# Kernel tuning notes

Hardware: AMD Instinct MI355X
Metric: run time of the kernel (lower is better)

## Reference

```python
import jax, jax.numpy as jnp
import numpy as np

B = 262144
N_USERS = 100000
N_LOCS = 2000
N_ISBNS = 100000
SBERT_DIM = 384
NUM_CATS = 64
EMB = 48
TEMP = 0.05
ALPHA = 3.0
BETA = 1.0


def setup_inputs() -> dict:
    key = jax.random.key(0)
    ks = jax.random.split(key, 20)
    s = 0.05
    inp = {
        "user_idx": jax.random.randint(ks[0], (B,), 0, N_USERS),
        "loc_idx": jax.random.randint(ks[1], (B,), 0, N_LOCS),
        "pos_idx": jax.random.randint(ks[2], (B,), 0, N_ISBNS),
        "neg_idx": jax.random.randint(ks[3], (B,), 0, N_ISBNS),
        "user_cat_emb": jax.random.normal(ks[4], (N_USERS, EMB), jnp.float32) * s,
        "user_txt_emb": jax.random.normal(ks[5], (N_USERS, EMB), jnp.float32) * s,
        "loc_cat_emb": jax.random.normal(ks[6], (N_LOCS, EMB), jnp.float32) * s,
        "loc_txt_emb": jax.random.normal(ks[7], (N_LOCS, EMB), jnp.float32) * s,
        "sbert_matrix": jax.random.normal(ks[8], (N_ISBNS, SBERT_DIM), jnp.float32) * s,
        # multi-hot category matrix (~3 categories per book on average)
        "book_cat_mh": (jax.random.uniform(ks[9], (N_ISBNS, NUM_CATS)) < 0.05).astype(jnp.float32),
        "Wc1": jax.random.normal(ks[10], (NUM_CATS, 128), jnp.float32) * s,
        "bc1": jnp.zeros((128,), jnp.float32),
        "Wc2": jax.random.normal(ks[11], (128, EMB), jnp.float32) * s,
        "bc2": jnp.zeros((EMB,), jnp.float32),
        "Wt1": jax.random.normal(ks[12], (SBERT_DIM, 256), jnp.float32) * s,
        "bt1": jnp.zeros((256,), jnp.float32),
        "Wt2": jax.random.normal(ks[13], (256, EMB), jnp.float32) * s,
        "bt2": jnp.zeros((EMB,), jnp.float32),
    }
    return inp


def _l2norm(x):
    # tf.nn.l2_normalize: x / sqrt(max(sum(x^2), eps)), eps=1e-12
    sq = jnp.sum(x * x, axis=-1, keepdims=True)
    return x * jax.lax.rsqrt(jnp.maximum(sq, 1e-12))


def _encode_book(idx, sbert_matrix, book_cat_mh, Wc1, bc1, Wc2, bc2, Wt1, bt1, Wt2, bt2):
    b_cat_in = book_cat_mh[idx]                      # [B, NUM_CATS]
    b_txt_in = sbert_matrix[idx]                     # [B, SBERT_DIM]
    b_cat = jax.nn.relu(b_cat_in @ Wc1 + bc1) @ Wc2 + bc2   # [B, EMB]
    b_txt = jax.nn.relu(b_txt_in @ Wt1 + bt1) @ Wt2 + bt2   # [B, EMB]
    return _l2norm(ALPHA * b_cat + BETA * b_txt)


def reference(user_idx, loc_idx, pos_idx, neg_idx,
              user_cat_emb, user_txt_emb, loc_cat_emb, loc_txt_emb,
              sbert_matrix, book_cat_mh,
              Wc1, bc1, Wc2, bc2, Wt1, bt1, Wt2, bt2):
    # user tower (dropout inactive at inference)
    u = ALPHA * (user_cat_emb[user_idx] + loc_cat_emb[loc_idx]) \
        + BETA * (user_txt_emb[user_idx] + loc_txt_emb[loc_idx])
    u = _l2norm(u)
    p = _encode_book(pos_idx, sbert_matrix, book_cat_mh, Wc1, bc1, Wc2, bc2, Wt1, bt1, Wt2, bt2)
    n = _encode_book(neg_idx, sbert_matrix, book_cat_mh, Wc1, bc1, Wc2, bc2, Wt1, bt1, Wt2, bt2)
    pos_sim = jnp.sum(u * p, axis=-1) / TEMP
    neg_sim = jnp.sum(u * n, axis=-1) / TEMP
    return jnp.stack([pos_sim, neg_sim], axis=-1)  # [B, 2]
```

## Files before the change

### kernel.cpp

```cpp
#include <hip/hip_runtime.h>

#define SBD   384
#define NCATS 64
#define EMB   48
#define HT    256
#define HC    128
#define MB    64

typedef __attribute__((ext_vector_type(8))) short short8;
typedef __attribute__((ext_vector_type(4))) float f32x4;

__device__ __forceinline__ short f2bf(float x) {
    union { float f; unsigned u; } v; v.f = x;
    unsigned r = v.u + 0x7FFF + ((v.u >> 16) & 1);
    return (short)(r >> 16);
}

__device__ __forceinline__ void glds16(const void* g, void* l) {
    __builtin_amdgcn_global_load_lds((const __attribute__((address_space(1))) void*)g,
                                     (__attribute__((address_space(3))) void*)l, 16, 0, 0);
}

__global__ void prep_weights(const float* __restrict__ Wt1, const float* __restrict__ Wt2,
                             const float* __restrict__ Wc1, const float* __restrict__ Wc2,
                             char* __restrict__ iT1, char* __restrict__ iT2,
                             char* __restrict__ iC1, char* __restrict__ iC2) {
    int t = blockIdx.x * blockDim.x + threadIdx.x;
    int stride = gridDim.x * blockDim.x;
    for (int g = t; g < 256 * 48; g += stride) {
        int n = g / 48, k0 = (g - n * 48) * 8;
        int c = k0 >> 5, kin = k0 & 31;
        short8 v;
        #pragma unroll
        for (int j = 0; j < 8; ++j) v[j] = f2bf(Wt1[(size_t)(k0 + j) * HT + n]);
        *(short8*)(iT1 + (size_t)c * 16384 + ((n * 64 + kin * 2) ^ ((n & 7) << 4))) = v;
    }
    for (int g = t; g < 48 * 32; g += stride) {
        int n = g / 32, k0 = (g - n * 32) * 8;
        short8 v;
        #pragma unroll
        for (int j = 0; j < 8; ++j) v[j] = f2bf(Wt2[(size_t)(k0 + j) * EMB + n]);
        *(short8*)(iT2 + ((n * 512 + k0 * 2) ^ ((n & 7) << 4))) = v;
    }
    for (int g = t; g < 128 * 8; g += stride) {
        int n = g / 8, k0 = (g - n * 8) * 8;
        short8 v;
        #pragma unroll
        for (int j = 0; j < 8; ++j) v[j] = f2bf(Wc1[(size_t)(k0 + j) * HC + n]);
        *(short8*)(iC1 + ((n * 128 + k0 * 2) ^ ((n & 7) << 4))) = v;
    }
    for (int g = t; g < 48 * 16; g += stride) {
        int n = g / 16, k0 = (g - n * 16) * 8;
        short8 v;
        #pragma unroll
        for (int j = 0; j < 8; ++j) v[j] = f2bf(Wc2[(size_t)(k0 + j) * EMB + n]);
        *(short8*)(iC2 + ((n * 256 + k0 * 2) ^ ((n & 7) << 4))) = v;
    }
}

__global__ __launch_bounds__(256, 2) void encode_books_mfma(
    const float* __restrict__ sbert, const float* __restrict__ mh,
    const char* __restrict__ iT1, const char* __restrict__ iT2,
    const char* __restrict__ iC1, const char* __restrict__ iC2,
    const float* __restrict__ bt1, const float* __restrict__ bt2,
    const float* __restrict__ bc1, const float* __restrict__ bc2,
    float* __restrict__ E, int nbooks)
{
    __shared__ char lds[73728];

    const int t  = threadIdx.x;
    const int w  = t >> 6;
    const int l  = t & 63;
    const int lr = l & 15;
    const int lg = l >> 4;
    const int book0 = blockIdx.x * MB;
    const int arow  = w * 16 + lr;
    const int drow0 = w * 16 + lg * 4;
    const int aswz  = (arow & 7) << 4;
    const int nswz  = (lr & 7) << 4;

    auto stageA = [&](int c, int buf) {
        int row = t >> 2, k0 = (t & 3) * 8;
        int rb = min(book0 + row, nbooks - 1);
        const float* s = sbert + (size_t)rb * SBD + c * 32 + k0;
        float4 v0 = *(const float4*)s, v1 = *(const float4*)(s + 4);
        short8 h;
        h[0] = f2bf(v0.x); h[1] = f2bf(v0.y); h[2] = f2bf(v0.z); h[3] = f2bf(v0.w);
        h[4] = f2bf(v1.x); h[5] = f2bf(v1.y); h[6] = f2bf(v1.z); h[7] = f2bf(v1.w);
        *(short8*)(lds + buf * 4096 + ((row * 64 + k0 * 2) ^ ((row & 7) << 4))) = h;
    };
    auto stageB = [&](const char* img, int dst, int bytes) {
        int perw = bytes >> 2;
        for (int i = 0; i < perw; i += 1024)
            glds16(img + w * perw + i + l * 16, lds + dst + w * perw + i);
    };

    f32x4 acc[16];
    #pragma unroll
    for (int nt = 0; nt < 16; ++nt) { float b = bt1[nt * 16 + lr]; acc[nt] = (f32x4){b, b, b, b}; }

    stageA(0, 0);
    stageB(iT1, 8192, 16384);
    __syncthreads();
    for (int c = 0; c < 12; ++c) {
        const int cur = c & 1;
        if (c < 11) {
            stageA(c + 1, cur ^ 1);
            stageB(iT1 + (size_t)(c + 1) * 16384, 8192 + (cur ^ 1) * 16384, 16384);
        }
        short8 af = *(const short8*)(lds + cur * 4096 + ((arow * 64 + lg * 16) ^ aswz));
        #pragma unroll
        for (int nt = 0; nt < 16; ++nt) {
            short8 bf = *(const short8*)(lds + 8192 + cur * 16384 +
                                         (((nt * 16 + lr) * 64 + lg * 16) ^ nswz));
            acc[nt] = __builtin_amdgcn_mfma_f32_16x16x32_bf16(af, bf, acc[nt], 0, 0, 0);
        }
        __syncthreads();
    }

    #pragma unroll
    for (int nt = 0; nt < 16; ++nt) {
        #pragma unroll
        for (int r = 0; r < 4; ++r) {
            int row = drow0 + r, col = nt * 16 + lr;
            *(unsigned short*)(lds + 40960 + ((row * 512 + col * 2) ^ ((row & 7) << 4))) =
                (unsigned short)f2bf(fmaxf(acc[nt][r], 0.f));
        }
    }
    stageB(iT2, 8192, 24576);
    #pragma unroll
    for (int i = 0; i < 2; ++i) {
        int g = t + 256 * i;
        int row = g >> 3, k0 = (g & 7) * 8;
        int rb = min(book0 + row, nbooks - 1);
        const float* s = mh + (size_t)rb * NCATS + k0;
        float4 v0 = *(const float4*)s, v1 = *(const float4*)(s + 4);
        short8 h;
        h[0] = f2bf(v0.x); h[1] = f2bf(v0.y); h[2] = f2bf(v0.z); h[3] = f2bf(v0.w);
        h[4] = f2bf(v1.x); h[5] = f2bf(v1.y); h[6] = f2bf(v1.z); h[7] = f2bf(v1.w);
        *(short8*)(lds + ((row * 128 + k0 * 2) ^ ((row & 7) << 4))) = h;
    }
    __syncthreads();

    f32x4 acct[3];
    #pragma unroll
    for (int nt = 0; nt < 3; ++nt) { float b = bt2[nt * 16 + lr]; acct[nt] = (f32x4){b, b, b, b}; }
    #pragma unroll
    for (int ks = 0; ks < 8; ++ks) {
        short8 af = *(const short8*)(lds + 40960 + ((arow * 512 + (lg * 8 + ks * 32) * 2) ^ aswz));
        #pragma unroll
        for (int nt = 0; nt < 3; ++nt) {
            short8 bf = *(const short8*)(lds + 8192 +
                (((nt * 16 + lr) * 512 + (lg * 8 + ks * 32) * 2) ^ nswz));
            acct[nt] = __builtin_amdgcn_mfma_f32_16x16x32_bf16(af, bf, acct[nt], 0, 0, 0);
        }
    }
    __syncthreads();

    stageB(iC1, 8192, 16384);
    stageB(iC2, 24576, 12288);
    __syncthreads();

    f32x4 accc[8];
    #pragma unroll
    for (int nt = 0; nt < 8; ++nt) { float b = bc1[nt * 16 + lr]; accc[nt] = (f32x4){b, b, b, b}; }
    #pragma unroll
    for (int ks = 0; ks < 2; ++ks) {
        short8 af = *(const short8*)(lds + ((arow * 128 + (lg * 8 + ks * 32) * 2) ^ aswz));
        #pragma unroll
        for (int nt = 0; nt < 8; ++nt) {
            short8 bf = *(const short8*)(lds + 8192 +
                (((nt * 16 + lr) * 128 + (lg * 8 + ks * 32) * 2) ^ nswz));
            accc[nt] = __builtin_amdgcn_mfma_f32_16x16x32_bf16(af, bf, accc[nt], 0, 0, 0);
        }
    }
    #pragma unroll
    for (int nt = 0; nt < 8; ++nt) {
        #pragma unroll
        for (int r = 0; r < 4; ++r) {
            int row = drow0 + r, col = nt * 16 + lr;
            *(unsigned short*)(lds + 40960 + ((row * 256 + col * 2) ^ ((row & 7) << 4))) =
                (unsigned short)f2bf(fmaxf(accc[nt][r], 0.f));
        }
    }
    __syncthreads();

    f32x4 acc2[3];
    #pragma unroll
    for (int nt = 0; nt < 3; ++nt) { float b = bc2[nt * 16 + lr]; acc2[nt] = (f32x4){b, b, b, b}; }
    #pragma unroll
    for (int ks = 0; ks < 4; ++ks) {
        short8 af = *(const short8*)(lds + 40960 + ((arow * 256 + (lg * 8 + ks * 32) * 2) ^ aswz));
        #pragma unroll
        for (int nt = 0; nt < 3; ++nt) {
            short8 bf = *(const short8*)(lds + 24576 +
                (((nt * 16 + lr) * 256 + (lg * 8 + ks * 32) * 2) ^ nswz));
            acc2[nt] = __builtin_amdgcn_mfma_f32_16x16x32_bf16(af, bf, acc2[nt], 0, 0, 0);
        }
    }

    f32x4 comb[3];
    #pragma unroll
    for (int nt = 0; nt < 3; ++nt)
        #pragma unroll
        for (int r = 0; r < 4; ++r) comb[nt][r] = 3.0f * acc2[nt][r] + acct[nt][r];
    float rn[4];
    #pragma unroll
    for (int r = 0; r < 4; ++r) {
        float ss = comb[0][r] * comb[0][r] + comb[1][r] * comb[1][r] + comb[2][r] * comb[2][r];
        ss += __shfl_xor(ss, 1); ss += __shfl_xor(ss, 2);
        ss += __shfl_xor(ss, 4); ss += __shfl_xor(ss, 8);
        rn[r] = rsqrtf(fmaxf(ss, 1e-12f));
    }
    #pragma unroll
    for (int nt = 0; nt < 3; ++nt) {
        #pragma unroll
        for (int r = 0; r < 4; ++r) {
            int grow = book0 + drow0 + r;
            if (grow < nbooks) E[(size_t)grow * EMB + nt * 16 + lr] = comb[nt][r] * rn[r];
        }
    }
}

__global__ __launch_bounds__(256) void score_kernel(
    const int* __restrict__ user_idx, const int* __restrict__ loc_idx,
    const int* __restrict__ pos_idx,  const int* __restrict__ neg_idx,
    const float* __restrict__ ucat, const float* __restrict__ utxt,
    const float* __restrict__ lcat, const float* __restrict__ ltxt,
    const float* __restrict__ E, float* __restrict__ out, int Bn)
{
    const int t    = threadIdx.x;
    const int lane = t & 15;
    const int s    = blockIdx.x * 16 + (t >> 4);
    if (s >= Bn) return;

    const int ui = user_idx[s];
    const int li = loc_idx[s];
    const int pi = pos_idx[s];
    const int ni = neg_idx[s];

    const int d0 = lane * 3;
    const float* uc = ucat + (size_t)ui * EMB + d0;
    const float* ut = utxt + (size_t)ui * EMB + d0;
    const float* lc = lcat + (size_t)li * EMB + d0;
    const float* lt = ltxt + (size_t)li * EMB + d0;
    const float* pp = E + (size_t)pi * EMB + d0;
    const float* nn = E + (size_t)ni * EMB + d0;

    float u0 = 3.0f * (uc[0] + lc[0]) + (ut[0] + lt[0]);
    float u1 = 3.0f * (uc[1] + lc[1]) + (ut[1] + lt[1]);
    float u2 = 3.0f * (uc[2] + lc[2]) + (ut[2] + lt[2]);

    float usq = u0 * u0 + u1 * u1 + u2 * u2;
    float ps  = u0 * pp[0] + u1 * pp[1] + u2 * pp[2];
    float ns  = u0 * nn[0] + u1 * nn[1] + u2 * nn[2];

    #pragma unroll
    for (int m = 1; m < 16; m <<= 1) {
        usq += __shfl_xor(usq, m);
        ps  += __shfl_xor(ps, m);
        ns  += __shfl_xor(ns, m);
    }

    if (lane == 0) {
        const float inv = rsqrtf(fmaxf(usq, 1e-12f)) * 20.0f;
        out[2 * (size_t)s + 0] = ps * inv;
        out[2 * (size_t)s + 1] = ns * inv;
    }
}

extern "C" void kernel_launch(void* const* d_in, const int* in_sizes, int n_in,
                              void* d_out, int out_size, void* d_ws, size_t ws_size,
                              hipStream_t stream) {
    const int*   user_idx = (const int*)d_in[0];
    const int*   loc_idx  = (const int*)d_in[1];
    const int*   pos_idx  = (const int*)d_in[2];
    const int*   neg_idx  = (const int*)d_in[3];
    const float* ucat     = (const float*)d_in[4];
    const float* utxt     = (const float*)d_in[5];
    const float* lcat     = (const float*)d_in[6];
    const float* ltxt     = (const float*)d_in[7];
    const float* sbert    = (const float*)d_in[8];
    const float* mh       = (const float*)d_in[9];
    const float* Wc1      = (const float*)d_in[10];
    const float* Wc2      = (const float*)d_in[12];
    const float* bc2      = (const float*)d_in[13];
    const float* bc1      = (const float*)d_in[11];
    const float* Wt1      = (const float*)d_in[14];
    const float* bt1      = (const float*)d_in[15];
    const float* Wt2      = (const float*)d_in[16];
    const float* bt2      = (const float*)d_in[17];

    const int Bn     = in_sizes[0];
    const int nbooks = in_sizes[8] / SBD;

    char* ws = (char*)d_ws;
    float* E = (float*)ws;
    size_t off = (size_t)nbooks * EMB * 4;
    off = (off + 255) & ~(size_t)255;
    char* iT1 = ws + off; off += 196608;
    char* iT2 = ws + off; off += 24576;
    char* iC1 = ws + off; off += 16384;
    char* iC2 = ws + off; off += 12288;

    hipLaunchKernelGGL(prep_weights, dim3(64), dim3(256), 0, stream,
                       Wt1, Wt2, Wc1, Wc2, iT1, iT2, iC1, iC2);

    const int nblocksA = (nbooks + MB - 1) / MB;
    hipLaunchKernelGGL(encode_books_mfma, dim3(nblocksA), dim3(256), 0, stream,
                       sbert, mh, iT1, iT2, iC1, iC2, bt1, bt2, bc1, bc2, E, nbooks);

    const int nblocksB = (Bn + 15) / 16;
    hipLaunchKernelGGL(score_kernel, dim3(nblocksB), dim3(256), 0, stream,
                       user_idx, loc_idx, pos_idx, neg_idx,
                       ucat, utxt, lcat, ltxt, E, (float*)d_out, Bn);
}
```

Baseline: 117.8 us.

## Load weight fragments directly from global into registers, retile first GEMM 2x2 across waves

Weight images are no longer staged into LDS through global_load_lds. MFMA B fragments are now read directly from global (L2/L1) into registers, with a double-buffered register prefetch for the Wt1 chunks and a deeper register prefetch for the sbert rows. The first GEMM is retiled so each wave computes a 32x128 block (2x8 MFMA tiles) rather than 16x256. This cuts LDS traffic and the number of barriers per chunk, and shrinks the LDS footprint. The cost is more VGPR pressure and reliance on cache hits for the small weight matrices in the later GEMMs.

```diff
diff --git a/kernel.cpp b/kernel.cpp
--- a/kernel.cpp
+++ b/kernel.cpp
@@ -16,9 +16,11 @@
     return (short)(r >> 16);
 }
 
-__device__ __forceinline__ void glds16(const void* g, void* l) {
-    __builtin_amdgcn_global_load_lds((const __attribute__((address_space(1))) void*)g,
-                                     (__attribute__((address_space(3))) void*)l, 16, 0, 0);
+__device__ __forceinline__ short8 cvt8(float4 a, float4 b) {
+    short8 h;
+    h[0] = f2bf(a.x); h[1] = f2bf(a.y); h[2] = f2bf(a.z); h[3] = f2bf(a.w);
+    h[4] = f2bf(b.x); h[5] = f2bf(b.y); h[6] = f2bf(b.z); h[7] = f2bf(b.w);
+    return h;
 }
 
 __global__ void prep_weights(const float* __restrict__ Wt1, const float* __restrict__ Wt2,
@@ -33,28 +35,28 @@
         short8 v;
         #pragma unroll
         for (int j = 0; j < 8; ++j) v[j] = f2bf(Wt1[(size_t)(k0 + j) * HT + n]);
-        *(short8*)(iT1 + (size_t)c * 16384 + ((n * 64 + kin * 2) ^ ((n & 7) << 4))) = v;
+        *(short8*)(iT1 + (size_t)c * 16384 + n * 64 + kin * 2) = v;
     }
     for (int g = t; g < 48 * 32; g += stride) {
         int n = g / 32, k0 = (g - n * 32) * 8;
         short8 v;
         #pragma unroll
         for (int j = 0; j < 8; ++j) v[j] = f2bf(Wt2[(size_t)(k0 + j) * EMB + n]);
-        *(short8*)(iT2 + ((n * 512 + k0 * 2) ^ ((n & 7) << 4))) = v;
+        *(short8*)(iT2 + n * 512 + k0 * 2) = v;
     }
     for (int g = t; g < 128 * 8; g += stride) {
         int n = g / 8, k0 = (g - n * 8) * 8;
         short8 v;
         #pragma unroll
         for (int j = 0; j < 8; ++j) v[j] = f2bf(Wc1[(size_t)(k0 + j) * HC + n]);
-        *(short8*)(iC1 + ((n * 128 + k0 * 2) ^ ((n & 7) << 4))) = v;
+        *(short8*)(iC1 + n * 128 + k0 * 2) = v;
     }
     for (int g = t; g < 48 * 16; g += stride) {
         int n = g / 16, k0 = (g - n * 16) * 8;
         short8 v;
         #pragma unroll
         for (int j = 0; j < 8; ++j) v[j] = f2bf(Wc2[(size_t)(k0 + j) * EMB + n]);
-        *(short8*)(iC2 + ((n * 256 + k0 * 2) ^ ((n & 7) << 4))) = v;
+        *(short8*)(iC2 + n * 256 + k0 * 2) = v;
     }
 }
 
@@ -66,7 +68,7 @@
     const float* __restrict__ bc1, const float* __restrict__ bc2,
     float* __restrict__ E, int nbooks)
 {
-    __shared__ char lds[73728];
+    __shared__ char lds[65536];
 
     const int t  = threadIdx.x;
     const int w  = t >> 6;
@@ -74,60 +76,79 @@
     const int lr = l & 15;
     const int lg = l >> 4;
     const int book0 = blockIdx.x * MB;
-    const int arow  = w * 16 + lr;
-    const int drow0 = w * 16 + lg * 4;
-    const int aswz  = (arow & 7) << 4;
-    const int nswz  = (lr & 7) << 4;
-
-    auto stageA = [&](int c, int buf) {
-        int row = t >> 2, k0 = (t & 3) * 8;
-        int rb = min(book0 + row, nbooks - 1);
-        const float* s = sbert + (size_t)rb * SBD + c * 32 + k0;
-        float4 v0 = *(const float4*)s, v1 = *(const float4*)(s + 4);
-        short8 h;
-        h[0] = f2bf(v0.x); h[1] = f2bf(v0.y); h[2] = f2bf(v0.z); h[3] = f2bf(v0.w);
-        h[4] = f2bf(v1.x); h[5] = f2bf(v1.y); h[6] = f2bf(v1.z); h[7] = f2bf(v1.w);
-        *(short8*)(lds + buf * 4096 + ((row * 64 + k0 * 2) ^ ((row & 7) << 4))) = h;
-    };
-    auto stageB = [&](const char* img, int dst, int bytes) {
-        int perw = bytes >> 2;
-        for (int i = 0; i < perw; i += 1024)
-            glds16(img + w * perw + i + l * 16, lds + dst + w * perw + i);
-    };
-
-    f32x4 acc[16];
-    #pragma unroll
-    for (int nt = 0; nt < 16; ++nt) { float b = bt1[nt * 16 + lr]; acc[nt] = (f32x4){b, b, b, b}; }
-
-    stageA(0, 0);
-    stageB(iT1, 8192, 16384);
-    __syncthreads();
+    const int wm = w >> 1, wn = w & 1;
+
+    const int srow = t >> 2, sk0 = (t & 3) * 8;
+    const int sdst = (srow * 64 + sk0 * 2) ^ ((srow & 7) << 4);
+    const size_t srb = (size_t)min(book0 + srow, nbooks - 1) * SBD + sk0;
+
+    const char* bb1 = iT1 + wn * 8192 + lr * 64 + lg * 16;
+
+    f32x4 acc[2][8];
+    #pragma unroll
+    for (int nt = 0; nt < 8; ++nt) {
+        float b = bt1[wn * 128 + nt * 16 + lr];
+        acc[0][nt] = (f32x4){b, b, b, b};
+        acc[1][nt] = (f32x4){b, b, b, b};
+    }
+
+    float4 ar[4][2];
+    short8 bb[2][8];
+
+    #pragma unroll
+    for (int c = 0; c < 3; ++c) {
+        const float* p = sbert + srb + c * 32;
+        ar[c][0] = *(const float4*)p;
+        ar[c][1] = *(const float4*)(p + 4);
+    }
+    #pragma unroll
+    for (int nt = 0; nt < 8; ++nt) bb[0][nt] = *(const short8*)(bb1 + nt * 1024);
+    *(short8*)(lds + sdst) = cvt8(ar[0][0], ar[0][1]);
+    asm volatile("s_waitcnt lgkmcnt(0)" ::: "memory");
+    __builtin_amdgcn_sched_barrier(0);
+    __builtin_amdgcn_s_barrier();
+
+    const int ar0 = wm * 32 + lr, ar1 = wm * 32 + 16 + lr;
+    const int aoff0 = (ar0 * 64 + lg * 16) ^ ((ar0 & 7) << 4);
+    const int aoff1 = (ar1 * 64 + lg * 16) ^ ((ar1 & 7) << 4);
+
+    #pragma unroll
     for (int c = 0; c < 12; ++c) {
-        const int cur = c & 1;
-        if (c < 11) {
-            stageA(c + 1, cur ^ 1);
-            stageB(iT1 + (size_t)(c + 1) * 16384, 8192 + (cur ^ 1) * 16384, 16384);
-        }
-        short8 af = *(const short8*)(lds + cur * 4096 + ((arow * 64 + lg * 16) ^ aswz));
-        #pragma unroll
-        for (int nt = 0; nt < 16; ++nt) {
-            short8 bf = *(const short8*)(lds + 8192 + cur * 16384 +
-                                         (((nt * 16 + lr) * 64 + lg * 16) ^ nswz));
-            acc[nt] = __builtin_amdgcn_mfma_f32_16x16x32_bf16(af, bf, acc[nt], 0, 0, 0);
-        }
-        __syncthreads();
-    }
-
-    #pragma unroll
-    for (int nt = 0; nt < 16; ++nt) {
-        #pragma unroll
-        for (int r = 0; r < 4; ++r) {
-            int row = drow0 + r, col = nt * 16 + lr;
-            *(unsigned short*)(lds + 40960 + ((row * 512 + col * 2) ^ ((row & 7) << 4))) =
-                (unsigned short)f2bf(fmaxf(acc[nt][r], 0.f));
-        }
-    }
-    stageB(iT2, 8192, 24576);
+        if (c + 1 < 12) {
+            #pragma unroll
+            for (int nt = 0; nt < 8; ++nt)
+                bb[(c + 1) & 1][nt] = *(const short8*)(bb1 + (c + 1) * 16384 + nt * 1024);
+        }
+        if (c + 3 < 12) {
+            const float* p = sbert + srb + (c + 3) * 32;
+            ar[(c + 3) & 3][0] = *(const float4*)p;
+            ar[(c + 3) & 3][1] = *(const float4*)(p + 4);
+        }
+        if (c + 1 < 12)
+            *(short8*)(lds + ((c + 1) & 1) * 4096 + sdst) = cvt8(ar[(c + 1) & 3][0], ar[(c + 1) & 3][1]);
+        short8 af0 = *(const short8*)(lds + (c & 1) * 4096 + aoff0);
+        short8 af1 = *(const short8*)(lds + (c & 1) * 4096 + aoff1);
+        #pragma unroll
+        for (int nt = 0; nt < 8; ++nt) {
+            acc[0][nt] = __builtin_amdgcn_mfma_f32_16x16x32_bf16(af0, bb[c & 1][nt], acc[0][nt], 0, 0, 0);
+            acc[1][nt] = __builtin_amdgcn_mfma_f32_16x16x32_bf16(af1, bb[c & 1][nt], acc[1][nt], 0, 0, 0);
+        }
+        asm volatile("s_waitcnt lgkmcnt(0)" ::: "memory");
+        __builtin_amdgcn_sched_barrier(0);
+        __builtin_amdgcn_s_barrier();
+    }
+
+    #pragma unroll
+    for (int mt = 0; mt < 2; ++mt)
+        #pragma unroll
+        for (int nt = 0; nt < 8; ++nt)
+            #pragma unroll
+            for (int r = 0; r < 4; ++r) {
+                int row = wm * 32 + mt * 16 + lg * 4 + r;
+                int col = wn * 128 + nt * 16 + lr;
+                *(unsigned short*)(lds + 8192 + ((row * 512 + col * 2) ^ ((row & 7) << 4))) =
+                    (unsigned short)f2bf(fmaxf(acc[mt][nt][r], 0.f));
+            }
     #pragma unroll
     for (int i = 0; i < 2; ++i) {
         int g = t + 256 * i;
@@ -135,66 +156,61 @@
         int rb = min(book0 + row, nbooks - 1);
         const float* s = mh + (size_t)rb * NCATS + k0;
         float4 v0 = *(const float4*)s, v1 = *(const float4*)(s + 4);
-        short8 h;
-        h[0] = f2bf(v0.x); h[1] = f2bf(v0.y); h[2] = f2bf(v0.z); h[3] = f2bf(v0.w);
-        h[4] = f2bf(v1.x); h[5] = f2bf(v1.y); h[6] = f2bf(v1.z); h[7] = f2bf(v1.w);
-        *(short8*)(lds + ((row * 128 + k0 * 2) ^ ((row & 7) << 4))) = h;
-    }
-    __syncthreads();
+        *(short8*)(lds + 40960 + ((row * 128 + k0 * 2) ^ ((row & 7) << 4))) = cvt8(v0, v1);
+    }
+    asm volatile("s_waitcnt lgkmcnt(0)" ::: "memory");
+    __builtin_amdgcn_sched_barrier(0);
+    __builtin_amdgcn_s_barrier();
+
+    const int arow = w * 16 + lr;
+    const int aswz = (lr & 7) << 4;
 
     f32x4 acct[3];
     #pragma unroll
     for (int nt = 0; nt < 3; ++nt) { float b = bt2[nt * 16 + lr]; acct[nt] = (f32x4){b, b, b, b}; }
     #pragma unroll
     for (int ks = 0; ks < 8; ++ks) {
-        short8 af = *(const short8*)(lds + 40960 + ((arow * 512 + (lg * 8 + ks * 32) * 2) ^ aswz));
+        short8 af = *(const short8*)(lds + 8192 + ((arow * 512 + (lg * 8 + ks * 32) * 2) ^ aswz));
         #pragma unroll
         for (int nt = 0; nt < 3; ++nt) {
-            short8 bf = *(const short8*)(lds + 8192 +
-                (((nt * 16 + lr) * 512 + (lg * 8 + ks * 32) * 2) ^ nswz));
+            short8 bf = *(const short8*)(iT2 + (nt * 16 + lr) * 512 + (lg * 8 + ks * 32) * 2);
             acct[nt] = __builtin_amdgcn_mfma_f32_16x16x32_bf16(af, bf, acct[nt], 0, 0, 0);
         }
     }
-    __syncthreads();
-
-    stageB(iC1, 8192, 16384);
-    stageB(iC2, 24576, 12288);
-    __syncthreads();
 
     f32x4 accc[8];
     #pragma unroll
     for (int nt = 0; nt < 8; ++nt) { float b = bc1[nt * 16 + lr]; accc[nt] = (f32x4){b, b, b, b}; }
     #pragma unroll
     for (int ks = 0; ks < 2; ++ks) {
-        short8 af = *(const short8*)(lds + ((arow * 128 + (lg * 8 + ks * 32) * 2) ^ aswz));
+        short8 af = *(const short8*)(lds + 40960 + ((arow * 128 + (lg * 8 + ks * 32) * 2) ^ aswz));
         #pragma unroll
         for (int nt = 0; nt < 8; ++nt) {
-            short8 bf = *(const short8*)(lds + 8192 +
-                (((nt * 16 + lr) * 128 + (lg * 8 + ks * 32) * 2) ^ nswz));
+            short8 bf = *(const short8*)(iC1 + (nt * 16 + lr) * 128 + (lg * 8 + ks * 32) * 2);
             accc[nt] = __builtin_amdgcn_mfma_f32_16x16x32_bf16(af, bf, accc[nt], 0, 0, 0);
         }
     }
     #pragma unroll
-    for (int nt = 0; nt < 8; ++nt) {
+    for (int nt = 0; nt < 8; ++nt)
         #pragma unroll
         for (int r = 0; r < 4; ++r) {
-            int row = drow0 + r, col = nt * 16 + lr;
-            *(unsigned short*)(lds + 40960 + ((row * 256 + col * 2) ^ ((row & 7) << 4))) =
+            int row = w * 16 + lg * 4 + r, col = nt * 16 + lr;
+            *(unsigned short*)(lds + 49152 + ((row * 256 + col * 2) ^ ((row & 7) << 4))) =
                 (unsigned short)f2bf(fmaxf(accc[nt][r], 0.f));
         }
-    }
-    __syncthreads();
+    asm volatile("s_waitcnt lgkmcnt(0)" ::: "memory");
+    __builtin_amdgcn_sched_barrier(0);
+    __builtin_amdgcn_s_barrier();
 
     f32x4 acc2[3];
     #pragma unroll
     for (int nt = 0; nt < 3; ++nt) { float b = bc2[nt * 16 + lr]; acc2[nt] = (f32x4){b, b, b, b}; }
     #pragma unroll
     for (int ks = 0; ks < 4; ++ks) {
-        short8 af = *(const short8*)(lds + 40960 + ((arow * 256 + (lg * 8 + ks * 32) * 2) ^ aswz));
+        short8 af = *(const short8*)(lds + 49152 + ((arow * 256 + (lg * 8 + ks * 32) * 2) ^ aswz));
         #pragma unroll
         for (int nt = 0; nt < 3; ++nt) {
-            short8 bf = *(const short8*)(lds + 24576 +
-                (((nt * 16 + lr) * 256 + (lg * 8 + ks * 32) * 2) ^ nswz));
+            short8 bf = *(const short8*)(iC2 + (nt * 16 + lr) * 256 + (lg * 8 + ks * 32) * 2);
             acc2[nt] = __builtin_amdgcn_mfma_f32_16x16x32_bf16(af, bf, acc2[nt], 0, 0, 0);
         }
     }
@@ -213,13 +229,12 @@
         rn[r] = rsqrtf(fmaxf(ss, 1e-12f));
     }
     #pragma unroll
-    for (int nt = 0; nt < 3; ++nt) {
+    for (int nt = 0; nt < 3; ++nt)
         #pragma unroll
         for (int r = 0; r < 4; ++r) {
-            int grow = book0 + drow0 + r;
+            int grow = book0 + w * 16 + lg * 4 + r;
             if (grow < nbooks) E[(size_t)grow * EMB + nt * 16 + lr] = comb[nt][r] * rn[r];
         }
-    }
 }
 
 __global__ __launch_bounds__(256) void score_kernel(
@@ -283,9 +298,9 @@
     const float* sbert    = (const float*)d_in[8];
     const float* mh       = (const float*)d_in[9];
     const float* Wc1      = (const float*)d_in[10];
+    const float* bc1      = (const float*)d_in[11];
     const float* Wc2      = (const float*)d_in[12];
     const float* bc2      = (const float*)d_in[13];
-    const float* bc1      = (const float*)d_in[11];
     const float* Wt1      = (const float*)d_in[14];
     const float* bt1      = (const float*)d_in[15];
     const float* Wt2      = (const float*)d_in[16];
```

Result: slower. 142.8 us (+21.2%).
